# Kernel optimization log

Hardware: AMD Instinct MI355X
Metric: run time of the kernel (lower is better)

Reference implementation:

```python
import jax, jax.numpy as jnp
import numpy as np

B, S, D = 2, 2048, 1024
H = 16
K = 21  # tisa_num_kernels
HD = D // H


def setup_inputs() -> dict:
    key = jax.random.key(0)
    ks = jax.random.split(key, 7)
    x = jax.random.normal(ks[0], (B, S, D), dtype=jnp.float32)
    # in_proj: Linear(d_model, 3*d_model, bias=False); stored as (D, 3D) for x @ w
    w_in = jax.random.normal(ks[1], (D, 3 * D), dtype=jnp.float32) * (1.0 / np.sqrt(D))
    # gate: Linear(d_model, 2*d_model) with bias
    w_gate = jax.random.normal(ks[2], (D, 2 * D), dtype=jnp.float32) * (1.0 / np.sqrt(D))
    b_gate = jnp.zeros((2 * D,), dtype=jnp.float32)
    # TISA kernel params, one set of K kernels per head
    amplitudes = jax.random.normal(ks[3], (H, K), dtype=jnp.float32) * 0.1
    sharpness = jax.random.uniform(ks[4], (H, K), dtype=jnp.float32, minval=0.05, maxval=0.3)
    max_fv, min_fv = S // 2, 5
    offsets = jax.random.uniform(ks[5], (H, K), dtype=jnp.float32, minval=-float(max_fv), maxval=float(max_fv))
    return {"x": x, "w_in": w_in, "w_gate": w_gate, "b_gate": b_gate,
            "amplitudes": amplitudes, "sharpness": sharpness, "offsets": offsets}


def _tisa_bias(amplitudes, sharpness, offsets, seq_len):
    # Translation-invariant: score depends only on relative position j - i.
    # Compute scores over the 2S-1 unique relative positions, then gather.
    rel = jnp.arange(-(seq_len - 1), seq_len, dtype=jnp.float32)  # (2S-1,)
    # (H, K, 2S-1)
    d = rel[None, None, :] - offsets[:, :, None]
    scores = amplitudes[:, :, None] * jnp.exp(-jnp.abs(sharpness)[:, :, None] * d * d)
    scores = scores.sum(axis=1)  # (H, 2S-1)
    idx = jnp.arange(seq_len)
    rel_idx = idx[None, :] - idx[:, None] + (seq_len - 1)  # (S, S) in [0, 2S-2]
    return scores[:, rel_idx]  # (H, S, S)


def reference(x, w_in, w_gate, b_gate, amplitudes, sharpness, offsets):
    b, s, d = x.shape
    proj = x @ w_in  # (B, S, 3D); layout: [k | v | q]
    k, v, q = jnp.split(proj, 3, axis=-1)

    def heads(t):  # (B, S, D) -> (B, H, S, HD)
        return t.reshape(b, s, H, HD).transpose(0, 2, 1, 3)

    q, k, v = heads(q), heads(k), heads(v)
    scale = 1.0 / jnp.sqrt(jnp.float32(HD))
    scores = jnp.einsum('bhqd,bhkd->bhqk', q, k) * scale  # (B, H, S, S)
    scores = scores + _tisa_bias(amplitudes, sharpness, offsets, s)[None]
    weights = jax.nn.softmax(scores, axis=-1)
    attn = jnp.einsum('bhqk,bhkd->bhqd', weights, v)  # (B, H, S, HD)
    out = attn.transpose(0, 2, 1, 3).reshape(b, s, d)  # (B, S, D)
    gated = out @ w_gate + b_gate  # (B, S, 2D)
    a, g = jnp.split(gated, 2, axis=-1)
    return a * jax.nn.sigmoid(g)
```

## Files before the change

kernel.cpp:

```cpp
#include <hip/hip_runtime.h>
#include <math.h>

#define B_   2
#define S_   2048
#define D_   1024
#define H_   16
#define K_   21
#define HD_  64
#define D3_  3072
#define D2_  2048
#define REL_ 4095

typedef __attribute__((ext_vector_type(8))) short bf16x8;
typedef __attribute__((ext_vector_type(8))) unsigned short u16x8;
typedef __attribute__((ext_vector_type(4))) float f32x4;

#define MFMA16(a, b, c) __builtin_amdgcn_mfma_f32_16x16x32_bf16((a), (b), (c), 0, 0, 0)

__device__ __forceinline__ unsigned short f2bf(float f) {
    union { float f; unsigned u; } v; v.f = f;
    return (unsigned short)((v.u + 0x7fffu + ((v.u >> 16) & 1u)) >> 16);
}
__device__ __forceinline__ float bf2f(unsigned short h) {
    union { unsigned u; float f; } v; v.u = ((unsigned)h) << 16;
    return v.f;
}
__device__ __forceinline__ float asf(unsigned u) {
    union { unsigned u; float f; } v; v.u = u; return v.f;
}
__device__ __forceinline__ unsigned cvtpk(float a, float b) {
    unsigned r;
    asm("v_cvt_pk_bf16_f32 %0, %1, %2" : "=v"(r) : "v"(a), "v"(b));
    return r;
}
#define SPLIT8(f, ph, pl)                                                      \
    {                                                                          \
        _Pragma("unroll")                                                      \
        for (int _t = 0; _t < 4; ++_t) ph.u[_t] = cvtpk(f[2*_t], f[2*_t+1]);   \
        _Pragma("unroll")                                                      \
        for (int _t = 0; _t < 4; ++_t) {                                       \
            float _h0 = asf(ph.u[_t] << 16);                                   \
            float _h1 = asf(ph.u[_t] & 0xffff0000u);                           \
            pl.u[_t] = cvtpk(f[2*_t] - _h0, f[2*_t+1] - _h1);                  \
        }                                                                      \
    }

__device__ __forceinline__ void gload16(const void* g, void* l) {
    __builtin_amdgcn_global_load_lds(
        (const __attribute__((address_space(1))) unsigned int*)g,
        (__attribute__((address_space(3))) unsigned int*)l, 16, 0, 0);
}

__global__ void tisa_bias_kernel(const float* __restrict__ amp,
                                 const float* __restrict__ shp,
                                 const float* __restrict__ off,
                                 float* __restrict__ bias_rel) {
    int idx = blockIdx.x * blockDim.x + threadIdx.x;
    if (idx >= H_ * REL_) return;
    int h = idx / REL_;
    int r = idx - h * REL_;
    float rel = (float)(r - (S_ - 1));
    float acc = 0.f;
    #pragma unroll
    for (int k = 0; k < K_; ++k) {
        float d = rel - off[h * K_ + k];
        acc = fmaf(amp[h * K_ + k], expf(-fabsf(shp[h * K_ + k]) * d * d), acc);
    }
    bias_rel[idx] = acc;
}

template<bool PERM>
__global__ __launch_bounds__(256) void convert_wT_kernel(
    const float* __restrict__ in, unsigned short* __restrict__ out, int Kd, int N)
{
    __shared__ float t[64][65];
    const int tid = threadIdx.x;
    const int k0 = blockIdx.y * 64;
    const int n0 = blockIdx.x * 64;
    {
        const int r  = tid >> 2;
        const int cq = (tid & 3) * 16;
        #pragma unroll
        for (int e = 0; e < 4; ++e) {
            float4 v = *(const float4*)&in[(size_t)(k0 + r) * N + n0 + cq + 4 * e];
            t[r][cq + 4 * e + 0] = v.x;
            t[r][cq + 4 * e + 1] = v.y;
            t[r][cq + 4 * e + 2] = v.z;
            t[r][cq + 4 * e + 3] = v.w;
        }
    }
    __syncthreads();
    {
        const int n  = tid >> 2;
        const int ks = (tid & 3) * 16;
        const int nkc = Kd >> 5;
        unsigned short hi[16], lo[16];
        #pragma unroll
        for (int i = 0; i < 16; ++i) {
            float v = t[ks + i][n];
            hi[i] = f2bf(v);
            lo[i] = f2bf(v - bf2f(hi[i]));
        }
        const int kg = k0 + ks;
        const int kc = kg >> 5;
        const int j0 = kg & 31;
        const int nsrc = n0 + n;
        const int dc = PERM ? ((nsrc < 1024) ? 2 * nsrc : 2 * (nsrc - 1024) + 1) : nsrc;
        unsigned short* op = out + (size_t)dc * (nkc * 64) + kc * 64;
        *(u16x8*)&op[j0]          = *(u16x8*)&hi[0];
        *(u16x8*)&op[j0 + 8]      = *(u16x8*)&hi[8];
        *(u16x8*)&op[32 + j0]     = *(u16x8*)&lo[0];
        *(u16x8*)&op[32 + j0 + 8] = *(u16x8*)&lo[8];
    }
}

template<bool ASPLIT, int EPI>
__global__ __launch_bounds__(256) void gemm_split_kernel(
    const void* Ap, const unsigned short* __restrict__ Bt,
    const float* __restrict__ bias, float* C,
    int N, int Kd, int lda, int ldc)
{
    __shared__ unsigned short Al[128 * 64];
    __shared__ unsigned short Bl[128 * 64];
    const int tid  = threadIdx.x;
    const int w    = tid >> 6;
    const int lane = tid & 63;
    const int c    = lane & 15;
    const int g    = lane >> 4;
    const int m0   = blockIdx.y * 128;
    const int n0   = blockIdx.x * 128;
    const int wrow = (w >> 1) * 64;
    const int wcol = (w & 1) * 64;
    const int nkc  = Kd >> 5;

    f32x4 acc[4][4];
    #pragma unroll
    for (int i = 0; i < 4; ++i)
        #pragma unroll
        for (int j = 0; j < 4; ++j) acc[i][j] = (f32x4){0.f, 0.f, 0.f, 0.f};

    const int srowB  = w * 8 + (lane >> 3);
    const int sslotB = lane & 7;

    for (int kc = 0; kc < nkc; ++kc) {
        if (ASPLIT) {
            #pragma unroll
            for (int i = 0; i < 4; ++i) {
                const int row = w * 32 + i * 8 + (lane >> 3);
                const char* src = (const char*)Ap + (size_t)(m0 + row) * lda
                                + kc * 128 + (((lane & 7) ^ (row & 7)) << 4);
                gload16(src, (char*)Al + w * 4096 + i * 1024);
            }
        } else {
            const int am  = tid >> 1;
            const int ah_ = tid & 1;
            const float* ap = (const float*)Ap + (size_t)(m0 + am) * lda + kc * 32 + ah_ * 16;
            float v[16];
            #pragma unroll
            for (int e = 0; e < 4; ++e)
                *(float4*)&v[4 * e] = *(const float4*)(ap + 4 * e);
            union { unsigned u[4]; bf16x8 v; } h0, l0, h1, l1;
            {
                const float* f = v;     SPLIT8(f, h0, l0);
            }
            {
                const float* f = v + 8; SPLIT8(f, h1, l1);
            }
            char* rowp = (char*)Al + am * 128;
            *(uint4*)(rowp + (((2 * ah_ + 0) ^ (am & 7)) << 4)) = *(uint4*)&h0.u[0];
            *(uint4*)(rowp + (((2 * ah_ + 1) ^ (am & 7)) << 4)) = *(uint4*)&h1.u[0];
            *(uint4*)(rowp + (((4 + 2 * ah_ + 0) ^ (am & 7)) << 4)) = *(uint4*)&l0.u[0];
            *(uint4*)(rowp + (((4 + 2 * ah_ + 1) ^ (am & 7)) << 4)) = *(uint4*)&l1.u[0];
        }
        #pragma unroll
        for (int i = 0; i < 4; ++i) {
            const int n = i * 32 + srowB;
            const unsigned short* src = Bt
                + ((size_t)(n0 + n) * nkc + kc) * 64 + ((sslotB ^ (n & 7)) << 3);
            gload16(src, (char*)Bl + i * 4096 + w * 1024);
        }
        __syncthreads();

        bf16x8 ah[4], al[4], bh[4], bl[4];
        #pragma unroll
        for (int f = 0; f < 4; ++f) {
            const int m = wrow + f * 16 + c;
            const char* rp = (const char*)Al + m * 128;
            ah[f] = *(const bf16x8*)(rp + (((g + 0) ^ (m & 7)) << 4));
            al[f] = *(const bf16x8*)(rp + (((g + 4) ^ (m & 7)) << 4));
            const int n = wcol + f * 16 + c;
            const char* rq = (const char*)Bl + n * 128;
            bh[f] = *(const bf16x8*)(rq + (((g + 0) ^ (n & 7)) << 4));
            bl[f] = *(const bf16x8*)(rq + (((g + 4) ^ (n & 7)) << 4));
        }
        #pragma unroll
        for (int mf = 0; mf < 4; ++mf)
            #pragma unroll
            for (int nf = 0; nf < 4; ++nf) {
                acc[mf][nf] = MFMA16(ah[mf], bh[nf], acc[mf][nf]);
                acc[mf][nf] = MFMA16(al[mf], bh[nf], acc[mf][nf]);
                acc[mf][nf] = MFMA16(ah[mf], bl[nf], acc[mf][nf]);
            }
        __syncthreads();
    }

    if (EPI == 1) {
        if (n0 < 1024) {
            #pragma unroll
            for (int mf = 0; mf < 4; ++mf)
                #pragma unroll
                for (int r = 0; r < 4; ++r) {
                    const int row = m0 + wrow + mf * 16 + g * 4 + r;
                    char* rowB = (char*)C + (size_t)row * 12288;
                    #pragma unroll
                    for (int nf = 0; nf < 4; ++nf) {
                        const int col = n0 + wcol + nf * 16 + c;
                        const float val = acc[mf][nf][r];
                        const unsigned short hi = f2bf(val);
                        *(unsigned short*)(rowB + 4096 + 2 * col) = hi;
                        *(unsigned short*)(rowB + 6144 + 2 * col) = f2bf(val - bf2f(hi));
                    }
                }
        } else if (n0 < 2048) {
            #pragma unroll
            for (int mf = 0; mf < 4; ++mf) {
                const int row0 = m0 + wrow + mf * 16 + g * 4;
                const int s2 = (row0 & 2047) * 2;
                const size_t ibase = (size_t)(row0 >> 11) * 1024;
                #pragma unroll
                for (int nf = 0; nf < 4; ++nf) {
                    const int d = n0 - 1024 + wcol + nf * 16 + c;
                    ushort4 hv, lv;
                    {
                        float v0 = acc[mf][nf][0], v1 = acc[mf][nf][1];
                        float v2 = acc[mf][nf][2], v3 = acc[mf][nf][3];
                        hv.x = f2bf(v0); lv.x = f2bf(v0 - bf2f(hv.x));
                        hv.y = f2bf(v1); lv.y = f2bf(v1 - bf2f(hv.y));
                        hv.z = f2bf(v2); lv.z = f2bf(v2 - bf2f(hv.z));
                        hv.w = f2bf(v3); lv.w = f2bf(v3 - bf2f(hv.w));
                    }
                    char* base = (char*)C + (ibase + d) * (size_t)24576 + s2;
                    *(ushort4*)base           = hv;
                    *(ushort4*)(base + 12288) = lv;
                }
            }
        } else {
            #pragma unroll
            for (int mf = 0; mf < 4; ++mf)
                #pragma unroll
                for (int r = 0; r < 4; ++r) {
                    const int row = m0 + wrow + mf * 16 + g * 4 + r;
                    float* cp = &C[(size_t)row * ldc + n0 + wcol + c];
                    #pragma unroll
                    for (int nf = 0; nf < 4; ++nf)
                        cp[nf * 16] = acc[mf][nf][r];
                }
        }
    } else {
        float bgs[4];
        #pragma unroll
        for (int nf = 0; nf < 4; ++nf) {
            const int jc = n0 + wcol + nf * 16 + c;
            bgs[nf] = bias[(jc & 1) ? (1024 + (jc >> 1)) : (jc >> 1)];
        }
        #pragma unroll
        for (int mf = 0; mf < 4; ++mf)
            #pragma unroll
            for (int r = 0; r < 4; ++r) {
                const int row = m0 + wrow + mf * 16 + g * 4 + r;
                #pragma unroll
                for (int nf = 0; nf < 4; ++nf) {
                    const int jc = n0 + wcol + nf * 16 + c;
                    const float val = acc[mf][nf][r] + bgs[nf];
                    const float part = __shfl_xor(val, 1);
                    if (!(c & 1))
                        C[(size_t)row * ldc + (jc >> 1)] = val / (1.f + __expf(-part));
                }
            }
    }
}

__global__ __launch_bounds__(512) void attn_mfma_kernel(
    const float* projf, char* projB, const float* __restrict__ bias_rel)
{
    __shared__ unsigned short KHI[4096], KLO[4096], VHI[4096], VLO[4096];
    __shared__ unsigned short PHI[4096], PLO[4096];
    __shared__ float bias_s[192];

    const int tid  = threadIdx.x;
    const int w    = tid >> 6;
    const int lane = tid & 63;
    const int c    = lane & 15;
    const int g    = lane >> 4;
    const int bid  = blockIdx.x;
    const int xcd  = bid & 7;
    const int slot = bid >> 3;
    const int qt   = slot & 15;
    const int p    = (slot >> 4) * 8 + xcd;
    const int h    = p >> 1;
    const int b    = p & 1;
    const int qbase = qt * 128;
    const size_t rowbase = (size_t)b * S_;
    const int q    = 16 * w + c;
    const int psw  = (q & 3) ^ ((q >> 2) & 1);

    bf16x8 Qhi[2], Qlo[2];
    {
        const float* qp = projf + (rowbase + qbase + q) * D3_ + 2 * D_ + h * HD_;
        #pragma unroll
        for (int ck = 0; ck < 2; ++ck) {
            float q8[8];
            *(float4*)&q8[0] = *(const float4*)(qp + ck * 32 + g * 8);
            *(float4*)&q8[4] = *(const float4*)(qp + ck * 32 + g * 8 + 4);
            union { unsigned u[4]; bf16x8 v; } ph, pl;
            const float* f = q8;
            SPLIT8(f, ph, pl);
            Qhi[ck] = ph.v;
            Qlo[ck] = pl.v;
        }
    }

    f32x4 o_acc[4];
    #pragma unroll
    for (int n = 0; n < 4; ++n) o_acc[n] = (f32x4){0.f, 0.f, 0.f, 0.f};
    float m_run = -INFINITY;
    float l_run = 0.f;

    const int srow = tid >> 3;
    const int gsl  = (tid & 7) ^ (srow & 7);
    uint4 rkh, rkl, rvh, rvl;
    float breg = 0.f;

#define LOADKV(ktv)                                                            \
    {                                                                          \
        const int kbase_ = (ktv) * 64;                                         \
        const char* ks = projB + (rowbase + kbase_ + srow) * (size_t)12288     \
                       + 4096 + h * 128 + gsl * 16;                            \
        rkh = *(const uint4*)ks;  rkl = *(const uint4*)(ks + 2048);            \
        const char* vs = projB + (size_t)(b * 1024 + h * HD_ + srow) * 24576   \
                       + (size_t)kbase_ * 2 + gsl * 16;                        \
        rvh = *(const uint4*)vs;  rvl = *(const uint4*)(vs + 12288);           \
        if (tid < 191)                                                         \
            breg = bias_rel[h * REL_ + kbase_ - qbase + 1920 + tid];           \
    }

    LOADKV(0);

    for (int kt = 0; kt < S_ / 64; ++kt) {
        __syncthreads();
        {
            const int d = srow * 128 + (tid & 7) * 16;
            *(uint4*)((char*)KHI + d) = rkh;
            *(uint4*)((char*)KLO + d) = rkl;
            *(uint4*)((char*)VHI + d) = rvh;
            *(uint4*)((char*)VLO + d) = rvl;
            if (tid < 191) bias_s[tid] = breg;
        }
        if (kt + 1 < S_ / 64) LOADKV(kt + 1);
        __syncthreads();

        f32x4 sf[4];
        __builtin_amdgcn_s_setprio(1);
        #pragma unroll
        for (int f = 0; f < 4; ++f) {
            f32x4 acc = (f32x4){0.f, 0.f, 0.f, 0.f};
            const int krow = f * 16 + c;
            const unsigned short* kbp = KHI + krow * 64;
            const unsigned short* klp = KLO + krow * 64;
            #pragma unroll
            for (int ck = 0; ck < 2; ++ck) {
                const int s = ((ck * 4 + g) ^ (krow & 7)) * 8;
                bf16x8 kh  = *(const bf16x8*)(kbp + s);
                bf16x8 kl8 = *(const bf16x8*)(klp + s);
                acc = MFMA16(kh, Qhi[ck], acc);
                acc = MFMA16(kl8, Qhi[ck], acc);
                acc = MFMA16(kh, Qlo[ck], acc);
            }
            sf[f] = acc;
        }
        __builtin_amdgcn_s_setprio(0);

        #pragma unroll
        for (int f = 0; f < 4; ++f) {
            const int tb = 16 * f + 4 * g - q + 127;
            #pragma unroll
            for (int r = 0; r < 4; ++r)
                sf[f][r] = fmaf(sf[f][r], 0.125f, bias_s[tb + r]);
        }

        float pm[4];
        #pragma unroll
        for (int f = 0; f < 4; ++f)
            pm[f] = fmaxf(fmaxf(sf[f][0], sf[f][1]), fmaxf(sf[f][2], sf[f][3]));
        float mt = fmaxf(fmaxf(pm[0], pm[1]), fmaxf(pm[2], pm[3]));
        mt = fmaxf(mt, __shfl_xor(mt, 16));
        mt = fmaxf(mt, __shfl_xor(mt, 32));
        if (!__all(mt <= m_run + 8.f)) {
            const float mn = fmaxf(m_run, mt);
            const float sc = __expf(m_run - mn);
            l_run *= sc;
            m_run = mn;
            #pragma unroll
            for (int r = 0; r < 4; ++r) {
                const float scr = __shfl(sc, 20 * g + r);
                #pragma unroll
                for (int n = 0; n < 4; ++n) o_acc[n][r] *= scr;
            }
        }
        float ps[4];
        #pragma unroll
        for (int f = 0; f < 4; ++f) {
            #pragma unroll
            for (int r = 0; r < 4; ++r)
                sf[f][r] = __expf(sf[f][r] - m_run);
            ps[f] = (sf[f][0] + sf[f][1]) + (sf[f][2] + sf[f][3]);
        }
        float rs = (ps[0] + ps[1]) + (ps[2] + ps[3]);
        rs += __shfl_xor(rs, 16);
        rs += __shfl_xor(rs, 32);
        l_run += rs;

        #pragma unroll
        for (int ck = 0; ck < 2; ++ck) {
            #pragma unroll
            for (int f2 = 0; f2 < 2; ++f2) {
                const int f = 2 * ck + f2;
                const unsigned uh0 = cvtpk(sf[f][0], sf[f][1]);
                const unsigned uh1 = cvtpk(sf[f][2], sf[f][3]);
                const float r0 = sf[f][0] - asf(uh0 << 16);
                const float r1 = sf[f][1] - asf(uh0 & 0xffff0000u);
                const float r2 = sf[f][2] - asf(uh1 << 16);
                const float r3 = sf[f][3] - asf(uh1 & 0xffff0000u);
                const unsigned ul0 = cvtpk(r0, r1);
                const unsigned ul1 = cvtpk(r2, r3);
                const int byte = q * 64
                    + ((((2 * f2 + (g >> 1)) ^ psw) << 4) + ((g & 1) << 3));
                uint2 vh2; vh2.x = uh0; vh2.y = uh1;
                uint2 vl2; vl2.x = ul0; vl2.y = ul1;
                *(uint2*)((char*)PHI + byte) = vh2;
                *(uint2*)((char*)PLO + byte) = vl2;
            }
            asm volatile("s_waitcnt lgkmcnt(0)" ::: "memory");
            const int rbyte = q * 64 + ((g ^ psw) << 4);
            bf16x8 pah = *(const bf16x8*)((char*)PHI + rbyte);
            bf16x8 pal = *(const bf16x8*)((char*)PLO + rbyte);
            __builtin_amdgcn_s_setprio(1);
            #pragma unroll
            for (int n = 0; n < 4; ++n) {
                const int d = 16 * n + c;
                const int s = ((ck * 4 + g) ^ (d & 7)) * 8;
                bf16x8 vh = *(const bf16x8*)(VHI + d * 64 + s);
                bf16x8 vl = *(const bf16x8*)(VLO + d * 64 + s);
                o_acc[n] = MFMA16(pah, vh, o_acc[n]);
                o_acc[n] = MFMA16(pal, vh, o_acc[n]);
                o_acc[n] = MFMA16(pah, vl, o_acc[n]);
            }
            __builtin_amdgcn_s_setprio(0);
        }
    }
#undef LOADKV

    const float inv = 1.f / l_run;
    #pragma unroll
    for (int r = 0; r < 4; ++r) {
        const float invr = __shfl(inv, 20 * g + r);
        unsigned short* op = (unsigned short*)(projB
            + (rowbase + qbase + 16 * w + 4 * g + r) * (size_t)12288 + 8192);
        #pragma unroll
        for (int n = 0; n < 4; ++n) {
            const float v = o_acc[n][r] * invr;
            const int col = h * HD_ + 16 * n + c;
            const int kc2 = col >> 5;
            const int j   = col & 31;
            const unsigned short hi = f2bf(v);
            op[kc2 * 64 + j]      = hi;
            op[kc2 * 64 + 32 + j] = f2bf(v - bf2f(hi));
        }
    }
}

extern "C" void kernel_launch(void* const* d_in, const int* in_sizes, int n_in,
                              void* d_out, int out_size, void* d_ws, size_t ws_size,
                              hipStream_t stream) {
    const float* x      = (const float*)d_in[0];
    const float* w_in   = (const float*)d_in[1];
    const float* w_gate = (const float*)d_in[2];
    const float* b_gate = (const float*)d_in[3];
    const float* amp    = (const float*)d_in[4];
    const float* shp    = (const float*)d_in[5];
    const float* off    = (const float*)d_in[6];
    float* outp = (float*)d_out;

    char* ws = (char*)d_ws;
    float*    proj     = (float*)ws;
    float*    bias_rel = (float*)(ws + 50331648);
    unsigned short* wT = (unsigned short*)(ws + 50331648 + 262144);

    tisa_bias_kernel<<<(H_ * REL_ + 255) / 256, 256, 0, stream>>>(amp, shp, off, bias_rel);
    convert_wT_kernel<false><<<dim3(D3_ / 64, D_ / 64), 256, 0, stream>>>(w_in, wT, D_, D3_);
    gemm_split_kernel<false, 1><<<dim3(D3_ / 128, (B_ * S_) / 128), 256, 0, stream>>>(
        x, wT, nullptr, proj, D3_, D_, D_, D3_);
    convert_wT_kernel<true><<<dim3(D2_ / 64, D_ / 64), 256, 0, stream>>>(w_gate, wT, D_, D2_);
    attn_mfma_kernel<<<512, 512, 0, stream>>>(proj, ws, bias_rel);
    gemm_split_kernel<true, 2><<<dim3(D2_ / 128, (B_ * S_) / 128), 256, 0, stream>>>(
        ws + 8192, wT, b_gate, outp, D2_, D_, 12288, D_);
}
```

Baseline: 288.9 us.

## Pre-split x to bf16 hi/lo once and remap GEMM blocks per XCD

Adds a kernel that converts x into a bf16 hi/lo split layout once, staged in the output buffer, so the first GEMM can use the same direct 16-byte global-to-LDS loads as the second GEMM. This removes the redundant fp32 load and split work each column block was repeating. The GEMM grid is also flattened to 1D and remapped so each XCD gets a contiguous band of N-columns, aiming at better L2 reuse of weight tiles. It adds an extra launch and an extra read and write of x.

```diff
diff --git a/kernel.cpp b/kernel.cpp
--- a/kernel.cpp
+++ b/kernel.cpp
@@ -69,6 +69,29 @@
     bias_rel[idx] = acc;
 }
 
+__global__ __launch_bounds__(256) void convert_x_kernel(
+    const float* __restrict__ in, unsigned short* __restrict__ out)
+{
+    const int t   = blockIdx.x * 256 + threadIdx.x;
+    const int row = t >> 7;
+    const int c8  = (t & 127) * 8;
+    const float* src = in + (size_t)row * D_ + c8;
+    float v[8];
+    *(float4*)&v[0] = *(const float4*)src;
+    *(float4*)&v[4] = *(const float4*)(src + 4);
+    unsigned short hi[8], lo[8];
+    #pragma unroll
+    for (int i = 0; i < 8; ++i) {
+        hi[i] = f2bf(v[i]);
+        lo[i] = f2bf(v[i] - bf2f(hi[i]));
+    }
+    const int kc = c8 >> 5;
+    const int j0 = c8 & 31;
+    unsigned short* op = out + (size_t)row * 2048 + kc * 64;
+    *(u16x8*)&op[j0]      = *(u16x8*)&hi[0];
+    *(u16x8*)&op[32 + j0] = *(u16x8*)&lo[0];
+}
+
 template<bool PERM>
 __global__ __launch_bounds__(256) void convert_wT_kernel(
     const float* __restrict__ in, unsigned short* __restrict__ out, int Kd, int N)
@@ -114,7 +137,7 @@
     }
 }
 
-template<bool ASPLIT, int EPI>
+template<int EPI>
 __global__ __launch_bounds__(256) void gemm_split_kernel(
     const void* Ap, const unsigned short* __restrict__ Bt,
     const float* __restrict__ bias, float* C,
@@ -127,8 +150,12 @@
     const int lane = tid & 63;
     const int c    = lane & 15;
     const int g    = lane >> 4;
-    const int m0   = blockIdx.y * 128;
-    const int n0   = blockIdx.x * 128;
+    const int bid = blockIdx.x;
+    const int cpx = (N >> 7) >> 3;
+    const int xcd = bid & 7;
+    const int s   = bid >> 3;
+    const int m0  = (s & 31) * 128;
+    const int n0  = (xcd * cpx + (s >> 5)) * 128;
     const int wrow = (w >> 1) * 64;
     const int wcol = (w & 1) * 64;
     const int nkc  = Kd >> 5;
@@ -143,34 +170,12 @@
     const int sslotB = lane & 7;
 
     for (int kc = 0; kc < nkc; ++kc) {
-        if (ASPLIT) {
-            #pragma unroll
-            for (int i = 0; i < 4; ++i) {
-                const int row = w * 32 + i * 8 + (lane >> 3);
-                const char* src = (const char*)Ap + (size_t)(m0 + row) * lda
-                                + kc * 128 + (((lane & 7) ^ (row & 7)) << 4);
-                gload16(src, (char*)Al + w * 4096 + i * 1024);
-            }
-        } else {
-            const int am  = tid >> 1;
-            const int ah_ = tid & 1;
-            const float* ap = (const float*)Ap + (size_t)(m0 + am) * lda + kc * 32 + ah_ * 16;
-            float v[16];
-            #pragma unroll
-            for (int e = 0; e < 4; ++e)
-                *(float4*)&v[4 * e] = *(const float4*)(ap + 4 * e);
-            union { unsigned u[4]; bf16x8 v; } h0, l0, h1, l1;
-            {
-                const float* f = v;     SPLIT8(f, h0, l0);
-            }
-            {
-                const float* f = v + 8; SPLIT8(f, h1, l1);
-            }
-            char* rowp = (char*)Al + am * 128;
-            *(uint4*)(rowp + (((2 * ah_ + 0) ^ (am & 7)) << 4)) = *(uint4*)&h0.u[0];
-            *(uint4*)(rowp + (((2 * ah_ + 1) ^ (am & 7)) << 4)) = *(uint4*)&h1.u[0];
-            *(uint4*)(rowp + (((4 + 2 * ah_ + 0) ^ (am & 7)) << 4)) = *(uint4*)&l0.u[0];
-            *(uint4*)(rowp + (((4 + 2 * ah_ + 1) ^ (am & 7)) << 4)) = *(uint4*)&l1.u[0];
+        #pragma unroll
+        for (int i = 0; i < 4; ++i) {
+            const int row = w * 32 + i * 8 + (lane >> 3);
+            const char* src = (const char*)Ap + (size_t)(m0 + row) * lda
+                            + kc * 128 + (((lane & 7) ^ (row & 7)) << 4);
+            gload16(src, (char*)Al + w * 4096 + i * 1024);
         }
         #pragma unroll
         for (int i = 0; i < 4; ++i) {
@@ -495,13 +500,15 @@
     float*    proj     = (float*)ws;
     float*    bias_rel = (float*)(ws + 50331648);
     unsigned short* wT = (unsigned short*)(ws + 50331648 + 262144);
+    unsigned short* xc = (unsigned short*)d_out;
 
     tisa_bias_kernel<<<(H_ * REL_ + 255) / 256, 256, 0, stream>>>(amp, shp, off, bias_rel);
+    convert_x_kernel<<<2048, 256, 0, stream>>>(x, xc);
     convert_wT_kernel<false><<<dim3(D3_ / 64, D_ / 64), 256, 0, stream>>>(w_in, wT, D_, D3_);
-    gemm_split_kernel<false, 1><<<dim3(D3_ / 128, (B_ * S_) / 128), 256, 0, stream>>>(
-        x, wT, nullptr, proj, D3_, D_, D_, D3_);
+    gemm_split_kernel<1><<<(D3_ / 128) * 32, 256, 0, stream>>>(
+        xc, wT, nullptr, proj, D3_, D_, 4096, D3_);
     convert_wT_kernel<true><<<dim3(D2_ / 64, D_ / 64), 256, 0, stream>>>(w_gate, wT, D_, D2_);
     attn_mfma_kernel<<<512, 512, 0, stream>>>(proj, ws, bias_rel);
-    gemm_split_kernel<true, 2><<<dim3(D2_ / 128, (B_ * S_) / 128), 256, 0, stream>>>(
+    gemm_split_kernel<2><<<(D2_ / 128) * 32, 256, 0, stream>>>(
         ws + 8192, wT, b_gate, outp, D2_, D_, 12288, D_);
 }
```

Measured after the change: 288.9 us. About the same (-0.0%).
